# Optimization experiments

Measured on AMD Instinct MI355X. Metric: run time of the kernel, lower is better.

## Reference

```python
import jax, jax.numpy as jnp
import numpy as np
from jax import lax

N, T, U, V = 32, 512, 100, 4096
BLANK = 0


def setup_inputs() -> dict:
    key = jax.random.key(0)
    k1, k2, k3, k4, k5 = jax.random.split(key, 5)
    encoder_out = jax.random.normal(k1, (N, T, V), dtype=jnp.float32)
    decoder_out = jax.random.normal(k2, (N, U + 1, V), dtype=jnp.float32)
    targets = jax.random.randint(k3, (N, U), 1, V)            # labels, never blank
    input_lengths = jax.random.randint(k4, (N,), T // 2, T + 1)
    target_lengths = jax.random.randint(k5, (N,), U // 2, U + 1)
    return {
        "encoder_out": encoder_out,
        "decoder_out": decoder_out,
        "targets": targets,
        "input_lengths": input_lengths,
        "target_lengths": target_lengths,
    }


def _logprob_single(enc, dec, y, in_len, tgt_len):
    # enc: (T, V)  dec: (U+1, V)  y: (U,)
    Um = y.shape[0]
    u_idx = jnp.arange(Um)
    # emit[t, u] = enc[t, y[u]] + dec[u, y[u]]  (cost of emitting label u+1 at time t)
    emit = enc[:, y] + dec[u_idx, y][None, :]          # (T, U)
    blank_e = enc[:, BLANK]                            # (T,)
    blank_d = dec[:, BLANK]                            # (U+1,)

    # t = 0 row: alpha[0, u] = sum_{k<u} emit[0, k]
    alpha0 = jnp.concatenate([jnp.zeros((1,), enc.dtype), jnp.cumsum(emit[0])])

    def row_step(alpha_prev, xs):
        be_prev, emit_t = xs
        # blank transition from row t-1 (same u)
        top = alpha_prev + be_prev + blank_d           # (U+1,)

        # label transition within row: alpha[u] = logaddexp(top[u], alpha[u-1] + emit_t[u-1])
        def u_step(carry, x):
            top_u, em = x
            a = jnp.logaddexp(top_u, carry + em)
            return a, a

        _, rest = lax.scan(u_step, top[0], (top[1:], emit_t))
        alpha = jnp.concatenate([top[:1], rest])
        return alpha, alpha

    _, rows = lax.scan(row_step, alpha0, (blank_e[:-1], emit[1:]))
    alphas = jnp.concatenate([alpha0[None, :], rows], axis=0)   # (T, U+1)

    # log p(y|x) = alpha[T-1, U] + enc[T-1, blank] + dec[U, blank] with true lengths
    return alphas[in_len - 1, tgt_len] + enc[in_len - 1, BLANK] + dec[tgt_len, BLANK]


def reference(encoder_out, decoder_out, targets, input_lengths, target_lengths):
    # reduction='none': returns per-utterance log p(y|x), shape (N,)
    return jax.vmap(_logprob_single)(encoder_out, decoder_out, targets,
                                     input_lengths, target_lengths)
```

## Files before the change

kernel.cpp:

```cpp
#include <hip/hip_runtime.h>

#define NB 32
#define TT 512
#define UU 100
#define UM 101
#define VV 4096
#define NEG (-1e30f)
#define WIN 64
#define L2E 1.4426950408889634f
#define LN2 0.6931471805599453f

__device__ __forceinline__ float vexp2(float x){ float r; asm("v_exp_f32 %0, %1" : "=v"(r) : "v"(x)); return r; }
__device__ __forceinline__ float vlog2(float x){ float r; asm("v_log_f32 %0, %1" : "=v"(r) : "v"(x)); return r; }

__device__ __forceinline__ float lae2(float a, float b) {
    float m  = fmaxf(a, b);
    float nd = fminf(a, b) - m;
    return m + vlog2(1.0f + vexp2(nd));
}

__global__ __launch_bounds__(128) void sort_k(const int* __restrict__ tgt,
                                              int* __restrict__ sy,
                                              int* __restrict__ su) {
    __shared__ int ky[128], pu[128];
    int n = blockIdx.x, tid = threadIdx.x;
    ky[tid] = (tid < UU) ? tgt[n * UU + tid] : 0x7FFFFFFF;
    pu[tid] = tid;
    __syncthreads();
    for (int k = 2; k <= 128; k <<= 1)
        for (int j = k >> 1; j > 0; j >>= 1) {
            int i = tid, ix = i ^ j;
            if (ix > i) {
                bool up = ((i & k) == 0);
                int a = ky[i], b = ky[ix];
                if ((a > b) == up) {
                    ky[i] = b; ky[ix] = a;
                    int tmp = pu[i]; pu[i] = pu[ix]; pu[ix] = tmp;
                }
            }
            __syncthreads();
        }
    sy[n * 128 + tid] = ky[tid];
    su[n * 128 + tid] = pu[tid];
}

__global__ __launch_bounds__(256) void gather_k(
        const float* __restrict__ enc, const int* __restrict__ ilen,
        const int* __restrict__ tlen, const int* __restrict__ sy,
        const int* __restrict__ su, float* __restrict__ em) {
    int tt = blockIdx.x, n = blockIdx.y;
    int tin = ilen[n], tg = tlen[n];
    int t0 = tt * 32;
    if (t0 >= tin) return;
    __shared__ float tile[32][104];
    __shared__ int syL[128], suL[128];
    int tid = threadIdx.x;
    if (tid < 128) { syL[tid] = sy[n * 128 + tid]; suL[tid] = su[n * 128 + tid]; }
    __syncthreads();
    const float* encn = enc + (size_t)n * TT * VV;
    int wave = tid >> 6, lane = tid & 63;

    float v[16];
#pragma unroll
    for (int it = 0; it < 8; ++it) {
        int t = t0 + wave * 8 + it;
        bool tok = (t < tin);
        int s1 = lane + 64;
        int j0 = suL[lane];
        int j1 = (s1 < 128) ? suL[s1] : 0;
        v[2 * it]     = NEG;
        v[2 * it + 1] = NEG;
        if (tok && j0 < tg)              v[2 * it]     = encn[(size_t)t * VV + syL[lane]] * L2E;
        if (tok && s1 < 100 && j1 < tg)  v[2 * it + 1] = encn[(size_t)t * VV + syL[s1]] * L2E;
    }
#pragma unroll
    for (int it = 0; it < 8; ++it) {
        int tl = wave * 8 + it;
        int s1 = lane + 64;
        tile[tl][suL[lane]] = v[2 * it];
        if (s1 < 100) tile[tl][suL[s1]] = v[2 * it + 1];
    }
    __syncthreads();
    for (int idx = tid; idx < UU * 32; idx += 256) {
        int j = idx >> 5, tl = idx & 31;
        em[((size_t)n * UU + j) * TT + t0 + tl] = tile[tl][j];
    }
}

__global__ __launch_bounds__(1024, 1) void dp_k(
        const float* __restrict__ enc, const float* __restrict__ dec,
        const int* __restrict__ tgt, const int* __restrict__ ilen,
        const int* __restrict__ tlen, const float* __restrict__ em,
        float* __restrict__ out) {
    __shared__ float emL[2][WIN][130];
    __shared__ float blkL[864];
    __shared__ float dvxL[UU];

    int n = blockIdx.x, tid = threadIdx.x;
    int tin = ilen[n], tg = tlen[n];
    int dend = tin - 1 + tg;
    int E = (dend + WIN - 1) / WIN;
    const float* encn = enc + (size_t)n * TT * VV;
    const float* decn = dec + (size_t)n * UM * VV;

    for (int i = tid; i < 864; i += 1024)
        blkL[i] = (i >= 128 && i < 128 + TT) ? encn[(size_t)(i - 128) * VV] * L2E : NEG;
    if (tid < UU) {
        int y = tgt[n * UU + tid];
        dvxL[tid] = decn[(size_t)tid * VV + y] * L2E;
    }
    __syncthreads();

    int wave = tid >> 6, lane = tid & 63;
    const float* emn = em + (size_t)n * UU * TT;

    auto FILLWIN = [&](int w, int base) {
        for (int r = wave - 1; r < 128; r += 15) {
            int u = (r < 100) ? (r + 1) : ((r == 100) ? 0 : r);
            int t = base + 1 + lane - u;
            float val = NEG;
            if (r < 100 && r < tg && t >= 0 && t < tin)
                val = emn[(size_t)r * TT + t] + dvxL[r];
            emL[w][lane][u] = val;
        }
    };

    if (wave != 0) FILLWIN(0, 0);

    bool fx16 = (lane == 16), fx32 = (lane == 32), fx48 = (lane == 48);
    bool cap0 = (2 * lane == tg), cap1 = (2 * lane + 1 == tg);
    float bd0 = decn[(size_t)min(2 * lane, UM - 1) * VV] * L2E;
    float bd1 = decn[(size_t)min(2 * lane + 1, UM - 1) * VV] * L2E;
    int ib0 = 127 - 2 * lane;
    float a0 = (lane == 0) ? 0.0f : NEG;
    float a1 = NEG;
    float res = NEG;

    float Re0[8], Re1[8], Rb0[8], Rb1[8], Se0[8], Se1[8], Sb0[8], Sb1[8];

    auto REFILL = [&](float (&e0)[8], float (&e1)[8], float (&b0)[8], float (&b1)[8],
                      const float* emb, int j0, int base) {
#pragma unroll
        for (int k = 0; k < 8; ++k) {
            int dm = j0 + k, d = base + 1 + dm;
            float2 ev = *(const float2*)(emb + dm * 130 + 2 * lane);
            e0[k] = ev.x; e1[k] = ev.y;
            b0[k] = blkL[ib0 + d] + bd0;
            b1[k] = blkL[ib0 + d - 1] + bd1;
        }
        __builtin_amdgcn_sched_barrier(0);
    };

    auto STEPS = [&](float (&e0)[8], float (&e1)[8], float (&b0)[8], float (&b1)[8],
                     int j0, int base) {
#pragma unroll
        for (int k = 0; k < 8; ++k) {
            int dd = base + 1 + j0 + k;
            int sh = __builtin_amdgcn_update_dpp(__float_as_int(NEG), __float_as_int(a1),
                                                 0x111, 0xF, 0xF, false);
            float s15 = __int_as_float(__builtin_amdgcn_readlane(__float_as_int(a1), 15));
            float s31 = __int_as_float(__builtin_amdgcn_readlane(__float_as_int(a1), 31));
            float s47 = __int_as_float(__builtin_amdgcn_readlane(__float_as_int(a1), 47));
            float l0 = __int_as_float(sh);
            l0 = fx16 ? s15 : l0;
            l0 = fx32 ? s31 : l0;
            l0 = fx48 ? s47 : l0;
            float bt0 = a0 + b0[k], et0 = l0 + e0[k];
            float bt1 = a1 + b1[k], et1 = a0 + e1[k];
            a0 = lae2(bt0, et0);
            a1 = lae2(bt1, et1);
            if (dd == dend) { if (cap0) res = a0; if (cap1) res = a1; }
        }
        __builtin_amdgcn_sched_barrier(0);
    };

    __syncthreads();

    for (int e = 0; e < E; ++e) {
        if (wave == 0) {
            int base = e * WIN;
            const float* emb = &emL[e & 1][0][0];
            REFILL(Re0, Re1, Rb0, Rb1, emb, 0, base);
            REFILL(Se0, Se1, Sb0, Sb1, emb, 8, base);  STEPS(Re0, Re1, Rb0, Rb1, 0, base);
            REFILL(Re0, Re1, Rb0, Rb1, emb, 16, base); STEPS(Se0, Se1, Sb0, Sb1, 8, base);
            REFILL(Se0, Se1, Sb0, Sb1, emb, 24, base); STEPS(Re0, Re1, Rb0, Rb1, 16, base);
            REFILL(Re0, Re1, Rb0, Rb1, emb, 32, base); STEPS(Se0, Se1, Sb0, Sb1, 24, base);
            REFILL(Se0, Se1, Sb0, Sb1, emb, 40, base); STEPS(Re0, Re1, Rb0, Rb1, 32, base);
            REFILL(Re0, Re1, Rb0, Rb1, emb, 48, base); STEPS(Se0, Se1, Sb0, Sb1, 40, base);
            REFILL(Se0, Se1, Sb0, Sb1, emb, 56, base); STEPS(Re0, Re1, Rb0, Rb1, 48, base);
            STEPS(Se0, Se1, Sb0, Sb1, 56, base);
        } else if (e + 1 < E) {
            FILLWIN((e + 1) & 1, (e + 1) * WIN);
        }
        __syncthreads();
    }

    if (wave == 0 && (cap0 | cap1)) {
        float fin  = blkL[128 + tin - 1];
        float bdtg = decn[(size_t)tg * VV] * L2E;
        out[n] = (res + fin + bdtg) * LN2;
    }
}

extern "C" void kernel_launch(void* const* d_in, const int* in_sizes, int n_in,
                              void* d_out, int out_size, void* d_ws, size_t ws_size,
                              hipStream_t hs) {
    const float* enc  = (const float*)d_in[0];
    const float* dec  = (const float*)d_in[1];
    const int*   tgt  = (const int*)d_in[2];
    const int*   ilen = (const int*)d_in[3];
    const int*   tlen = (const int*)d_in[4];
    float* out = (float*)d_out;

    float* em = (float*)d_ws;
    int*   sy = (int*)(em + (size_t)NB * UU * TT);
    int*   su = sy + NB * 128;

    hipLaunchKernelGGL(sort_k,   dim3(NB), dim3(128), 0, hs, tgt, sy, su);
    hipLaunchKernelGGL(gather_k, dim3(16, NB), dim3(256), 0, hs,
                       enc, ilen, tlen, sy, su, em);
    hipLaunchKernelGGL(dp_k,     dim3(NB), dim3(1024), 0, hs,
                       enc, dec, tgt, ilen, tlen, em, out);
}
```

Measured before the change: 78.04 us.

## Stream full encoder rows through LDS in gather and drop sort kernel

Removes the per-utterance bitonic sort kernel. The gather kernel now reads whole encoder rows with coalesced float4 loads, double-buffered in registers, stages each row in LDS, and picks out the target labels and blank column from there. It also writes the blank column to a compact buffer, so the DP kernel no longer does strided global reads of enc[:,0]. The cost is that the full encoder tensor (about 256 MB) is read instead of scattered sampled elements, plus two barriers per row. The tg masking of emissions is dropped, but masked values were unused.

Result: slower. 90.05 us (+15.4%).

```diff
diff --git a/kernel.cpp b/kernel.cpp
--- a/kernel.cpp
+++ b/kernel.cpp
@@ -19,76 +19,66 @@
     return m + vlog2(1.0f + vexp2(nd));
 }
 
-__global__ __launch_bounds__(128) void sort_k(const int* __restrict__ tgt,
-                                              int* __restrict__ sy,
-                                              int* __restrict__ su) {
-    __shared__ int ky[128], pu[128];
-    int n = blockIdx.x, tid = threadIdx.x;
-    ky[tid] = (tid < UU) ? tgt[n * UU + tid] : 0x7FFFFFFF;
-    pu[tid] = tid;
+__global__ __launch_bounds__(256) void gather_k(
+        const float* __restrict__ enc, const int* __restrict__ tgt,
+        const int* __restrict__ ilen,
+        float* __restrict__ em, float* __restrict__ blk) {
+    int tt = blockIdx.x, n = blockIdx.y;
+    int tin = ilen[n];
+    int t0 = tt * 32;
+    if (t0 >= tin) return;
+    int rows = min(32, tin - t0);
+
+    __shared__ float rowL[VV];
+    __shared__ float tile[32][105];
+    __shared__ float blkT[32];
+    __shared__ int   yL[UU];
+
+    int tid = threadIdx.x;
+    if (tid < UU) yL[tid] = tgt[n * UU + tid];
+    const float* encn = enc + (size_t)n * TT * VV;
+
+    float4 vA0, vA1, vA2, vA3, vB0, vB1, vB2, vB3;
+    {
+        const float4* rp = (const float4*)(encn + (size_t)t0 * VV);
+        vA0 = rp[tid]; vA1 = rp[tid + 256]; vA2 = rp[tid + 512]; vA3 = rp[tid + 768];
+    }
     __syncthreads();
-    for (int k = 2; k <= 128; k <<= 1)
-        for (int j = k >> 1; j > 0; j >>= 1) {
-            int i = tid, ix = i ^ j;
-            if (ix > i) {
-                bool up = ((i & k) == 0);
-                int a = ky[i], b = ky[ix];
-                if ((a > b) == up) {
-                    ky[i] = b; ky[ix] = a;
-                    int tmp = pu[i]; pu[i] = pu[ix]; pu[ix] = tmp;
-                }
+
+    float4* rl = (float4*)rowL;
+    for (int r = 0; r < rows; r += 2) {
+        rl[tid] = vA0; rl[tid + 256] = vA1; rl[tid + 512] = vA2; rl[tid + 768] = vA3;
+        if (r + 1 < rows) {
+            const float4* rp = (const float4*)(encn + (size_t)(t0 + r + 1) * VV);
+            vB0 = rp[tid]; vB1 = rp[tid + 256]; vB2 = rp[tid + 512]; vB3 = rp[tid + 768];
+        }
+        __syncthreads();
+        if (tid < UU)  tile[r][tid] = rowL[yL[tid]] * L2E;
+        if (tid == UU) blkT[r] = rowL[0] * L2E;
+        __syncthreads();
+        if (r + 1 < rows) {
+            rl[tid] = vB0; rl[tid + 256] = vB1; rl[tid + 512] = vB2; rl[tid + 768] = vB3;
+            if (r + 2 < rows) {
+                const float4* rp = (const float4*)(encn + (size_t)(t0 + r + 2) * VV);
+                vA0 = rp[tid]; vA1 = rp[tid + 256]; vA2 = rp[tid + 512]; vA3 = rp[tid + 768];
             }
             __syncthreads();
-        }
-    sy[n * 128 + tid] = ky[tid];
-    su[n * 128 + tid] = pu[tid];
-}
-
-__global__ __launch_bounds__(256) void gather_k(
-        const float* __restrict__ enc, const int* __restrict__ ilen,
-        const int* __restrict__ tlen, const int* __restrict__ sy,
-        const int* __restrict__ su, float* __restrict__ em) {
-    int tt = blockIdx.x, n = blockIdx.y;
-    int tin = ilen[n], tg = tlen[n];
-    int t0 = tt * 32;
-    if (t0 >= tin) return;
-    __shared__ float tile[32][104];
-    __shared__ int syL[128], suL[128];
-    int tid = threadIdx.x;
-    if (tid < 128) { syL[tid] = sy[n * 128 + tid]; suL[tid] = su[n * 128 + tid]; }
-    __syncthreads();
-    const float* encn = enc + (size_t)n * TT * VV;
-    int wave = tid >> 6, lane = tid & 63;
-
-    float v[16];
-#pragma unroll
-    for (int it = 0; it < 8; ++it) {
-        int t = t0 + wave * 8 + it;
-        bool tok = (t < tin);
-        int s1 = lane + 64;
-        int j0 = suL[lane];
-        int j1 = (s1 < 128) ? suL[s1] : 0;
-        v[2 * it]     = NEG;
-        v[2 * it + 1] = NEG;
-        if (tok && j0 < tg)              v[2 * it]     = encn[(size_t)t * VV + syL[lane]] * L2E;
-        if (tok && s1 < 100 && j1 < tg)  v[2 * it + 1] = encn[(size_t)t * VV + syL[s1]] * L2E;
-    }
-#pragma unroll
-    for (int it = 0; it < 8; ++it) {
-        int tl = wave * 8 + it;
-        int s1 = lane + 64;
-        tile[tl][suL[lane]] = v[2 * it];
-        if (s1 < 100) tile[tl][suL[s1]] = v[2 * it + 1];
-    }
-    __syncthreads();
+            if (tid < UU)  tile[r + 1][tid] = rowL[yL[tid]] * L2E;
+            if (tid == UU) blkT[r + 1] = rowL[0] * L2E;
+            __syncthreads();
+        }
+    }
+
     for (int idx = tid; idx < UU * 32; idx += 256) {
         int j = idx >> 5, tl = idx & 31;
-        em[((size_t)n * UU + j) * TT + t0 + tl] = tile[tl][j];
-    }
+        if (tl < rows)
+            em[((size_t)n * UU + j) * TT + t0 + tl] = tile[tl][j];
+    }
+    if (tid < rows) blk[n * TT + t0 + tid] = blkT[tid];
 }
 
 __global__ __launch_bounds__(1024, 1) void dp_k(
-        const float* __restrict__ enc, const float* __restrict__ dec,
+        const float* __restrict__ blk, const float* __restrict__ dec,
         const int* __restrict__ tgt, const int* __restrict__ ilen,
         const int* __restrict__ tlen, const float* __restrict__ em,
         float* __restrict__ out) {
@@ -100,11 +90,10 @@
     int tin = ilen[n], tg = tlen[n];
     int dend = tin - 1 + tg;
     int E = (dend + WIN - 1) / WIN;
-    const float* encn = enc + (size_t)n * TT * VV;
     const float* decn = dec + (size_t)n * UM * VV;
 
     for (int i = tid; i < 864; i += 1024)
-        blkL[i] = (i >= 128 && i < 128 + TT) ? encn[(size_t)(i - 128) * VV] * L2E : NEG;
+        blkL[i] = (i >= 128 && i < 128 + TT) ? blk[n * TT + (i - 128)] : NEG;
     if (tid < UU) {
         int y = tgt[n * UU + tid];
         dvxL[tid] = decn[(size_t)tid * VV + y] * L2E;
@@ -212,13 +201,11 @@
     const int*   tlen = (const int*)d_in[4];
     float* out = (float*)d_out;
 
-    float* em = (float*)d_ws;
-    int*   sy = (int*)(em + (size_t)NB * UU * TT);
-    int*   su = sy + NB * 128;
-
-    hipLaunchKernelGGL(sort_k,   dim3(NB), dim3(128), 0, hs, tgt, sy, su);
+    float* em  = (float*)d_ws;
+    float* blk = em + (size_t)NB * UU * TT;
+
     hipLaunchKernelGGL(gather_k, dim3(16, NB), dim3(256), 0, hs,
-                       enc, ilen, tlen, sy, su, em);
-    hipLaunchKernelGGL(dp_k,     dim3(NB), dim3(1024), 0, hs,
-                       enc, dec, tgt, ilen, tlen, em, out);
-}
+                       enc, tgt, ilen, em, blk);
+    hipLaunchKernelGGL(dp_k, dim3(NB), dim3(1024), 0, hs,
+                       blk, dec, tgt, ilen, tlen, em, out);
+}
```
